# Optimization experiments

Measured on AMD Instinct MI355X. Metric: run time of the kernel, lower is better.

## Reference

```python
import jax, jax.numpy as jnp
import numpy as np

B, I, H = 32768, 128, 128


def setup_inputs() -> dict:
    key = jax.random.key(0)
    ks = jax.random.split(key, 11)
    s = 1.0 / np.sqrt(H)
    return {
        "x": jax.random.normal(ks[0], (B, I), jnp.float32),
        "h": jax.random.normal(ks[1], (B, H), jnp.float32),
        "c": jax.random.normal(ks[2], (B, H), jnp.float32),
        "W1": jax.random.normal(ks[3], (H, I + H), jnp.float32) * s,
        "b1": jax.random.normal(ks[4], (H,), jnp.float32) * s + 1.0,  # forget-gate bias offset 1.0
        "W2": jax.random.normal(ks[5], (H, I + H), jnp.float32) * s,
        "b2": jax.random.normal(ks[6], (H,), jnp.float32) * s,
        "Wf": jax.random.normal(ks[7], (H, I + H), jnp.float32) * s,
        "bf": jax.random.normal(ks[8], (H,), jnp.float32) * s,
        "W3": jax.random.normal(ks[9], (H, I + H), jnp.float32) * s,
        "b3": jax.random.normal(ks[10], (H,), jnp.float32) * s,
    }


def reference(x, h, c, W1, b1, W2, b2, Wf, bf, W3, b3):
    # total_in = inp + hidden (coordinate-list concat == feature concat)
    total = jnp.concatenate([x, h], axis=-1)  # [B, I+H]
    sig1 = jax.nn.sigmoid(total @ W1.T + b1)  # forget gate (bias offset +1)
    sig2 = jax.nn.sigmoid(total @ W2.T + b2)  # input gate
    f_l = jnp.tanh(total @ Wf.T + bf)         # candidate via symmetric f
    sig3 = jax.nn.sigmoid(total @ W3.T + b3)  # output gate
    new_c = c * sig1 + sig2 * f_l             # fused elementwise combine
    new_h = jnp.tanh(new_c) * sig3
    return new_h, new_c
```

## Files before the change

### kernel.cpp

```cpp
#include <hip/hip_runtime.h>

#define B_TOTAL 32768
#define NROWB   128
#define TILE    32
#define NT      4

typedef __attribute__((ext_vector_type(8)))  short    bf16x8;
typedef __attribute__((ext_vector_type(4)))  float    f32x4;
typedef __attribute__((ext_vector_type(4)))  unsigned u32x4;

__device__ __forceinline__ unsigned rne1(float f) {
    unsigned u = __builtin_bit_cast(unsigned, f);
    return (u + 0x7FFFu + ((u >> 16) & 1u)) >> 16;
}
__device__ __forceinline__ unsigned cvtpk(float lo, float hi) {
    unsigned r;
    asm("v_cvt_pk_bf16_f32 %0, %1, %2" : "=v"(r) : "v"(lo), "v"(hi));
    return r;
}
__device__ __forceinline__ float fsig(float v) {
    return __fdividef(1.0f, 1.0f + __expf(-v));
}
__device__ __forceinline__ float ftanh(float v) {
    return 1.0f - __fdividef(2.0f, 1.0f + __expf(2.0f * v));
}

__global__ void wconv_kernel(const float* __restrict__ w1, const float* __restrict__ w2,
                             const float* __restrict__ wf, const float* __restrict__ w3,
                             u32x4* __restrict__ out) {
    int T = blockIdx.x * 256 + threadIdx.x;
    int F = T >> 6, l = T & 63;
    int cs = F >> 5, g = (F >> 3) & 3, ks = F & 7;
    const float* W = (g == 0) ? w1 : (g == 1) ? w2 : (g == 2) ? wf : w3;
    const float* s = W + (cs * 16 + (l & 15)) * 256 + ks * 32 + (l >> 4) * 8;
    f32x4 lo = *(const f32x4*)s;
    f32x4 hi = *(const f32x4*)(s + 4);
    u32x4 r;
    r[0] = rne1(lo[0]) | (rne1(lo[1]) << 16);
    r[1] = rne1(lo[2]) | (rne1(lo[3]) << 16);
    r[2] = rne1(hi[0]) | (rne1(hi[1]) << 16);
    r[3] = rne1(hi[2]) | (rne1(hi[3]) << 16);
    out[T] = r;
}

__global__ __launch_bounds__(256, 2) void lstm_kernel(
    const float* __restrict__ x, const float* __restrict__ h, const float* __restrict__ c,
    const bf16x8* __restrict__ wfrag,
    const float* __restrict__ b1, const float* __restrict__ b2,
    const float* __restrict__ bfv, const float* __restrict__ b3,
    float* __restrict__ out)
{
    __shared__ __align__(16) char smem[2][TILE * 1024];

    const int tid  = threadIdx.x;
    const int wave = tid >> 6;
    const int lane = tid & 63;
    const int cg   = blockIdx.x & 1;
    const long row0 = (long)(blockIdx.x >> 1) * NROWB;
    const int cs   = cg * 4 + wave;
    const int rb   = lane & 15;
    const int gcol4 = cs * 16 + (lane >> 4) * 4;

    auto STAGE = [&](int t) {
        char* buf = smem[t & 1];
        const long gr0 = row0 + (long)t * TILE;
#pragma unroll
        for (int i = 0; i < 8; ++i) {
            const int r = wave * 8 + i;
            const unsigned kb = ((unsigned)lane * 16u) ^ (((unsigned)r & 7u) << 4);
            const float* src = (kb < 512u)
                ? (x + (gr0 + r) * 128 + (kb >> 2))
                : (h + (gr0 + r) * 128 + ((kb - 512u) >> 2));
            __builtin_amdgcn_global_load_lds(
                (const __attribute__((address_space(1))) unsigned*)src,
                (__attribute__((address_space(3))) unsigned*)(buf + r * 1024),
                16, 0, 0);
        }
    };

    STAGE(0);

    bf16x8 wfr[4][8];
#pragma unroll
    for (int g = 0; g < 4; ++g)
#pragma unroll
        for (int ks = 0; ks < 8; ++ks)
            wfr[g][ks] = wfrag[(size_t)(cs * 32 + g * 8 + ks) * 64 + lane];

    f32x4 bias[4];
    bias[0] = *(const f32x4*)(b1 + gcol4);
    bias[1] = *(const f32x4*)(b2 + gcol4);
    bias[2] = *(const f32x4*)(bfv + gcol4);
    bias[3] = *(const f32x4*)(b3 + gcol4);

    float* out_h = out;
    float* out_c = out + (size_t)B_TOTAL * 128;

#pragma unroll 1
    for (int t = 0; t < NT; ++t) {
        __syncthreads();
        if (t + 1 < NT) STAGE(t + 1);

        const char* buf = smem[t & 1];
        const long gr0 = row0 + (long)t * TILE;

        f32x4 cv[2];
#pragma unroll
        for (int mt = 0; mt < 2; ++mt)
            cv[mt] = *(const f32x4*)(c + (gr0 + mt * 16 + rb) * 128 + gcol4);

        f32x4 acc[2][4];
#pragma unroll
        for (int mt = 0; mt < 2; ++mt)
#pragma unroll
            for (int g = 0; g < 4; ++g)
                acc[mt][g] = (f32x4){0.f, 0.f, 0.f, 0.f};

#pragma unroll
        for (int ks = 0; ks < 8; ++ks) {
            bf16x8 af[2];
#pragma unroll
            for (int mt = 0; mt < 2; ++mt) {
                const int r = mt * 16 + rb;
                const unsigned swz = ((unsigned)r & 7u) << 4;
                const unsigned kb  = (unsigned)(ks * 128 + (lane >> 4) * 32);
                const char* p = buf + r * 1024;
                f32x4 a0 = *(const f32x4*)(p + (kb ^ swz));
                f32x4 a1 = *(const f32x4*)(p + ((kb + 16u) ^ swz));
                union { unsigned u[4]; bf16x8 v; } pk;
                pk.u[0] = cvtpk(a0[0], a0[1]);
                pk.u[1] = cvtpk(a0[2], a0[3]);
                pk.u[2] = cvtpk(a1[0], a1[1]);
                pk.u[3] = cvtpk(a1[2], a1[3]);
                af[mt] = pk.v;
            }
#pragma unroll
            for (int g = 0; g < 4; ++g) {
                acc[0][g] = __builtin_amdgcn_mfma_f32_16x16x32_bf16(wfr[g][ks], af[0], acc[0][g], 0, 0, 0);
                acc[1][g] = __builtin_amdgcn_mfma_f32_16x16x32_bf16(wfr[g][ks], af[1], acc[1][g], 0, 0, 0);
            }
        }

#pragma unroll
        for (int mt = 0; mt < 2; ++mt) {
            f32x4 nh, nc;
#pragma unroll
            for (int j = 0; j < 4; ++j) {
                const float g1 = fsig(acc[mt][0][j] + bias[0][j]);
                const float g2 = fsig(acc[mt][1][j] + bias[1][j]);
                const float gf = ftanh(acc[mt][2][j] + bias[2][j]);
                const float g3 = fsig(acc[mt][3][j] + bias[3][j]);
                nc[j] = cv[mt][j] * g1 + g2 * gf;
                nh[j] = ftanh(nc[j]) * g3;
            }
            const long o = (gr0 + mt * 16 + rb) * 128 + gcol4;
            *(f32x4*)(out_h + o) = nh;
            *(f32x4*)(out_c + o) = nc;
        }
    }
}

extern "C" void kernel_launch(void* const* d_in, const int* in_sizes, int n_in,
                              void* d_out, int out_size, void* d_ws, size_t ws_size,
                              hipStream_t stream) {
    (void)in_sizes; (void)n_in; (void)out_size; (void)ws_size;
    const float* x  = (const float*)d_in[0];
    const float* h  = (const float*)d_in[1];
    const float* c  = (const float*)d_in[2];
    const float* W1 = (const float*)d_in[3];
    const float* b1 = (const float*)d_in[4];
    const float* W2 = (const float*)d_in[5];
    const float* b2 = (const float*)d_in[6];
    const float* Wf = (const float*)d_in[7];
    const float* bf = (const float*)d_in[8];
    const float* W3 = (const float*)d_in[9];
    const float* b3 = (const float*)d_in[10];

    wconv_kernel<<<64, 256, 0, stream>>>(W1, W2, Wf, W3, (u32x4*)d_ws);
    lstm_kernel<<<B_TOTAL / NROWB * 2, 256, 0, stream>>>(
        x, h, c, (const bf16x8*)d_ws, b1, b2, bf, b3, (float*)d_out);
}
```

Measured before the change: 36.22 us.

## Use 512-thread blocks covering all columns with 16-row tiles

```diff
diff --git a/kernel.cpp b/kernel.cpp
--- a/kernel.cpp
+++ b/kernel.cpp
@@ -1,8 +1,8 @@
 #include <hip/hip_runtime.h>
 
 #define B_TOTAL 32768
-#define NROWB   128
-#define TILE    32
+#define NROWB   64
+#define TILE    16
 #define NT      4
 
 typedef __attribute__((ext_vector_type(8)))  short    bf16x8;
@@ -43,7 +43,7 @@
     out[T] = r;
 }
 
-__global__ __launch_bounds__(256, 2) void lstm_kernel(
+__global__ __launch_bounds__(512, 4) void lstm_kernel(
     const float* __restrict__ x, const float* __restrict__ h, const float* __restrict__ c,
     const bf16x8* __restrict__ wfrag,
     const float* __restrict__ b1, const float* __restrict__ b2,
@@ -55,18 +55,16 @@
     const int tid  = threadIdx.x;
     const int wave = tid >> 6;
     const int lane = tid & 63;
-    const int cg   = blockIdx.x & 1;
-    const long row0 = (long)(blockIdx.x >> 1) * NROWB;
-    const int cs   = cg * 4 + wave;
-    const int rb   = lane & 15;
-    const int gcol4 = cs * 16 + (lane >> 4) * 4;
+    const long row0 = (long)blockIdx.x * NROWB;
+    const int rb    = lane & 15;
+    const int gcol4 = wave * 16 + (lane >> 4) * 4;
 
     auto STAGE = [&](int t) {
         char* buf = smem[t & 1];
         const long gr0 = row0 + (long)t * TILE;
 #pragma unroll
-        for (int i = 0; i < 8; ++i) {
-            const int r = wave * 8 + i;
+        for (int i = 0; i < 2; ++i) {
+            const int r = wave * 2 + i;
             const unsigned kb = ((unsigned)lane * 16u) ^ (((unsigned)r & 7u) << 4);
             const float* src = (kb < 512u)
                 ? (x + (gr0 + r) * 128 + (kb >> 2))
@@ -85,7 +83,7 @@
     for (int g = 0; g < 4; ++g)
 #pragma unroll
         for (int ks = 0; ks < 8; ++ks)
-            wfr[g][ks] = wfrag[(size_t)(cs * 32 + g * 8 + ks) * 64 + lane];
+            wfr[g][ks] = wfrag[(size_t)(wave * 32 + g * 8 + ks) * 64 + lane];
 
     f32x4 bias[4];
     bias[0] = *(const f32x4*)(b1 + gcol4);
@@ -99,64 +97,48 @@
 #pragma unroll 1
     for (int t = 0; t < NT; ++t) {
         __syncthreads();
+
+        const long gr0 = row0 + (long)t * TILE;
+        f32x4 cv = *(const f32x4*)(c + (gr0 + rb) * 128 + gcol4);
+
         if (t + 1 < NT) STAGE(t + 1);
 
         const char* buf = smem[t & 1];
-        const long gr0 = row0 + (long)t * TILE;
 
-        f32x4 cv[2];
+        f32x4 acc[4];
 #pragma unroll
-        for (int mt = 0; mt < 2; ++mt)
-            cv[mt] = *(const f32x4*)(c + (gr0 + mt * 16 + rb) * 128 + gcol4);
-
-        f32x4 acc[2][4];
-#pragma unroll
-        for (int mt = 0; mt < 2; ++mt)
-#pragma unroll
-            for (int g = 0; g < 4; ++g)
-                acc[mt][g] = (f32x4){0.f, 0.f, 0.f, 0.f};
+        for (int g = 0; g < 4; ++g) acc[g] = (f32x4){0.f, 0.f, 0.f, 0.f};
 
 #pragma unroll
         for (int ks = 0; ks < 8; ++ks) {
-            bf16x8 af[2];
+            const unsigned swz = ((unsigned)rb & 7u) << 4;
+            const unsigned kb  = (unsigned)(ks * 128 + (lane >> 4) * 32);
+            const char* p = buf + rb * 1024;
+            f32x4 a0 = *(const f32x4*)(p + (kb ^ swz));
+            f32x4 a1 = *(const f32x4*)(p + ((kb + 16u) ^ swz));
+            union { unsigned u[4]; bf16x8 v; } pk;
+            pk.u[0] = cvtpk(a0[0], a0[1]);
+            pk.u[1] = cvtpk(a0[2], a0[3]);
+            pk.u[2] = cvtpk(a1[0], a1[1]);
+            pk.u[3] = cvtpk(a1[2], a1[3]);
 #pragma unroll
-            for (int mt = 0; mt < 2; ++mt) {
-                const int r = mt * 16 + rb;
-                const unsigned swz = ((unsigned)r & 7u) << 4;
-                const unsigned kb  = (unsigned)(ks * 128 + (lane >> 4) * 32);
-                const char* p = buf + r * 1024;
-                f32x4 a0 = *(const f32x4*)(p + (kb ^ swz));
-                f32x4 a1 = *(const f32x4*)(p + ((kb + 16u) ^ swz));
-                union { unsigned u[4]; bf16x8 v; } pk;
-                pk.u[0] = cvtpk(a0[0], a0[1]);
-                pk.u[1] = cvtpk(a0[2], a0[3]);
-                pk.u[2] = cvtpk(a1[0], a1[1]);
-                pk.u[3] = cvtpk(a1[2], a1[3]);
-                af[mt] = pk.v;
-            }
-#pragma unroll
-            for (int g = 0; g < 4; ++g) {
-                acc[0][g] = __builtin_amdgcn_mfma_f32_16x16x32_bf16(wfr[g][ks], af[0], acc[0][g], 0, 0, 0);
-                acc[1][g] = __builtin_amdgcn_mfma_f32_16x16x32_bf16(wfr[g][ks], af[1], acc[1][g], 0, 0, 0);
-            }
+            for (int g = 0; g < 4; ++g)
+                acc[g] = __builtin_amdgcn_mfma_f32_16x16x32_bf16(wfr[g][ks], pk.v, acc[g], 0, 0, 0);
         }
 
+        f32x4 nh, nc;
 #pragma unroll
-        for (int mt = 0; mt < 2; ++mt) {
-            f32x4 nh, nc;
-#pragma unroll
-            for (int j = 0; j < 4; ++j) {
-                const float g1 = fsig(acc[mt][0][j] + bias[0][j]);
-                const float g2 = fsig(acc[mt][1][j] + bias[1][j]);
-                const float gf = ftanh(acc[mt][2][j] + bias[2][j]);
-                const float g3 = fsig(acc[mt][3][j] + bias[3][j]);
-                nc[j] = cv[mt][j] * g1 + g2 * gf;
-                nh[j] = ftanh(nc[j]) * g3;
-            }
-            const long o = (gr0 + mt * 16 + rb) * 128 + gcol4;
-            *(f32x4*)(out_h + o) = nh;
-            *(f32x4*)(out_c + o) = nc;
+        for (int j = 0; j < 4; ++j) {
+            const float g1 = fsig(acc[0][j] + bias[0][j]);
+            const float g2 = fsig(acc[1][j] + bias[1][j]);
+            const float gf = ftanh(acc[2][j] + bias[2][j]);
+            const float g3 = fsig(acc[3][j] + bias[3][j]);
+            nc[j] = cv[j] * g1 + g2 * gf;
+            nh[j] = ftanh(nc[j]) * g3;
         }
+        const long o = (gr0 + rb) * 128 + gcol4;
+        *(f32x4*)(out_h + o) = nh;
+        *(f32x4*)(out_c + o) = nc;
     }
 }
 
@@ -177,6 +159,6 @@
     const float* b3 = (const float*)d_in[10];
 
     wconv_kernel<<<64, 256, 0, stream>>>(W1, W2, Wf, W3, (u32x4*)d_ws);
-    lstm_kernel<<<B_TOTAL / NROWB * 2, 256, 0, stream>>>(
+    lstm_kernel<<<B_TOTAL / NROWB, 512, 0, stream>>>(
         x, h, c, (const bf16x8*)d_ws, b1, b2, bf, b3, (float*)d_out);
 }
```

After: 78.16 us. +115.8%, slower.

## Use 512-thread blocks covering all columns with prefetched c and partial waitcnt

Applied to the files above, without the earlier changes.

```diff
diff --git a/kernel.cpp b/kernel.cpp
--- a/kernel.cpp
+++ b/kernel.cpp
@@ -1,9 +1,9 @@
 #include <hip/hip_runtime.h>
 
 #define B_TOTAL 32768
-#define NROWB   128
+#define NROWB   256
 #define TILE    32
-#define NT      4
+#define NT      8
 
 typedef __attribute__((ext_vector_type(8)))  short    bf16x8;
 typedef __attribute__((ext_vector_type(4)))  float    f32x4;
@@ -43,7 +43,7 @@
     out[T] = r;
 }
 
-__global__ __launch_bounds__(256, 2) void lstm_kernel(
+__global__ __launch_bounds__(512, 2) void lstm_kernel(
     const float* __restrict__ x, const float* __restrict__ h, const float* __restrict__ c,
     const bf16x8* __restrict__ wfrag,
     const float* __restrict__ b1, const float* __restrict__ b2,
@@ -55,18 +55,17 @@
     const int tid  = threadIdx.x;
     const int wave = tid >> 6;
     const int lane = tid & 63;
-    const int cg   = blockIdx.x & 1;
-    const long row0 = (long)(blockIdx.x >> 1) * NROWB;
-    const int cs   = cg * 4 + wave;
     const int rb   = lane & 15;
-    const int gcol4 = cs * 16 + (lane >> 4) * 4;
+    const int c4   = lane >> 4;
+    const long row0 = (long)blockIdx.x * NROWB;
+    const int gcol4 = wave * 16 + c4 * 4;
 
-    auto STAGE = [&](int t) {
-        char* buf = smem[t & 1];
-        const long gr0 = row0 + (long)t * TILE;
+    auto STAGE = [&](int b, int tc) {
+        char* buf = smem[b & 1];
+        const long gr0 = row0 + (long)tc * TILE;
 #pragma unroll
-        for (int i = 0; i < 8; ++i) {
-            const int r = wave * 8 + i;
+        for (int i = 0; i < 4; ++i) {
+            const int r = wave * 4 + i;
             const unsigned kb = ((unsigned)lane * 16u) ^ (((unsigned)r & 7u) << 4);
             const float* src = (kb < 512u)
                 ? (x + (gr0 + r) * 128 + (kb >> 2))
@@ -78,14 +77,14 @@
         }
     };
 
-    STAGE(0);
+    STAGE(0, 0);
 
     bf16x8 wfr[4][8];
 #pragma unroll
     for (int g = 0; g < 4; ++g)
 #pragma unroll
         for (int ks = 0; ks < 8; ++ks)
-            wfr[g][ks] = wfrag[(size_t)(cs * 32 + g * 8 + ks) * 64 + lane];
+            wfr[g][ks] = wfrag[(size_t)(wave * 32 + g * 8 + ks) * 64 + lane];
 
     f32x4 bias[4];
     bias[0] = *(const f32x4*)(b1 + gcol4);
@@ -93,28 +92,29 @@
     bias[2] = *(const f32x4*)(bfv + gcol4);
     bias[3] = *(const f32x4*)(b3 + gcol4);
 
+    f32x4 cv0 = *(const f32x4*)(c + (row0 + rb) * 128 + gcol4);
+    f32x4 cv1 = *(const f32x4*)(c + (row0 + 16 + rb) * 128 + gcol4);
+
     float* out_h = out;
     float* out_c = out + (size_t)B_TOTAL * 128;
 
 #pragma unroll 1
     for (int t = 0; t < NT; ++t) {
-        __syncthreads();
-        if (t + 1 < NT) STAGE(t + 1);
+        asm volatile("s_waitcnt vmcnt(6)" ::: "memory");
+        __builtin_amdgcn_s_barrier();
+        __builtin_amdgcn_sched_barrier(0);
+
+        const int tn = (t + 1 < NT) ? (t + 1) : (NT - 1);
+        STAGE(t + 1, tn);
+        f32x4 ncv0 = *(const f32x4*)(c + (row0 + (long)tn * TILE + rb) * 128 + gcol4);
+        f32x4 ncv1 = *(const f32x4*)(c + (row0 + (long)tn * TILE + 16 + rb) * 128 + gcol4);
 
         const char* buf = smem[t & 1];
         const long gr0 = row0 + (long)t * TILE;
 
-        f32x4 cv[2];
-#pragma unroll
-        for (int mt = 0; mt < 2; ++mt)
-            cv[mt] = *(const f32x4*)(c + (gr0 + mt * 16 + rb) * 128 + gcol4);
-
         f32x4 acc[2][4];
 #pragma unroll
-        for (int mt = 0; mt < 2; ++mt)
-#pragma unroll
-            for (int g = 0; g < 4; ++g)
-                acc[mt][g] = (f32x4){0.f, 0.f, 0.f, 0.f};
+        for (int g = 0; g < 4; ++g) { acc[0][g] = bias[g]; acc[1][g] = bias[g]; }
 
 #pragma unroll
         for (int ks = 0; ks < 8; ++ks) {
@@ -123,7 +123,7 @@
             for (int mt = 0; mt < 2; ++mt) {
                 const int r = mt * 16 + rb;
                 const unsigned swz = ((unsigned)r & 7u) << 4;
-                const unsigned kb  = (unsigned)(ks * 128 + (lane >> 4) * 32);
+                const unsigned kb  = (unsigned)(ks * 128 + c4 * 32);
                 const char* p = buf + r * 1024;
                 f32x4 a0 = *(const f32x4*)(p + (kb ^ swz));
                 f32x4 a1 = *(const f32x4*)(p + ((kb + 16u) ^ swz));
@@ -143,20 +143,24 @@
 
 #pragma unroll
         for (int mt = 0; mt < 2; ++mt) {
+            const f32x4 cv = mt ? cv1 : cv0;
             f32x4 nh, nc;
 #pragma unroll
             for (int j = 0; j < 4; ++j) {
-                const float g1 = fsig(acc[mt][0][j] + bias[0][j]);
-                const float g2 = fsig(acc[mt][1][j] + bias[1][j]);
-                const float gf = ftanh(acc[mt][2][j] + bias[2][j]);
-                const float g3 = fsig(acc[mt][3][j] + bias[3][j]);
-                nc[j] = cv[mt][j] * g1 + g2 * gf;
+                const float g1 = fsig(acc[mt][0][j]);
+                const float g2 = fsig(acc[mt][1][j]);
+                const float gf = ftanh(acc[mt][2][j]);
+                const float g3 = fsig(acc[mt][3][j]);
+                nc[j] = cv[j] * g1 + g2 * gf;
                 nh[j] = ftanh(nc[j]) * g3;
             }
             const long o = (gr0 + mt * 16 + rb) * 128 + gcol4;
             *(f32x4*)(out_h + o) = nh;
             *(f32x4*)(out_c + o) = nc;
         }
+
+        cv0 = ncv0;
+        cv1 = ncv1;
     }
 }
 
@@ -177,6 +181,6 @@
     const float* b3 = (const float*)d_in[10];
 
     wconv_kernel<<<64, 256, 0, stream>>>(W1, W2, Wf, W3, (u32x4*)d_ws);
-    lstm_kernel<<<B_TOTAL / NROWB * 2, 256, 0, stream>>>(
+    lstm_kernel<<<B_TOTAL / NROWB, 512, 0, stream>>>(
         x, h, c, (const bf16x8*)d_ws, b1, b2, bf, b3, (float*)d_out);
 }
```

Measured after the change: 52.02 us. 43.6% more time.
